# Optimization experiments

Measured on AMD Instinct MI355X. Metric: run time of the kernel, lower is better.

Reference implementation:

```python
import jax, jax.numpy as jnp
import numpy as np

N_NODES = 1_000_000
N_EDGES = 16_000_000


def _mean_aggregate(x, src, dst, num_nodes):
    # PyG message passing: message x_j = x[src], mean-aggregated at dst.
    msgs = x[src]  # [E, d]
    sums = jax.ops.segment_sum(msgs, dst, num_segments=num_nodes)
    cnt = jax.ops.segment_sum(jnp.ones((src.shape[0],), x.dtype), dst,
                              num_segments=num_nodes)
    return sums / jnp.maximum(cnt, 1.0)[:, None]


def _sage_conv(x, src, dst, W_l, b_l, W_r, num_nodes):
    # PyG SAGEConv (aggr='mean'): out = lin_l(mean_j x_j) + lin_r(x_i)
    agg = _mean_aggregate(x, src, dst, num_nodes)
    return agg @ W_l + b_l + x @ W_r


def setup_inputs() -> dict:
    key = jax.random.key(0)
    ks = jax.random.split(key, 12)
    x = jax.random.normal(ks[0], (N_NODES, 1), dtype=jnp.float32)
    edge_index = jax.random.randint(ks[1], (2, N_EDGES), 0, N_NODES, dtype=jnp.int64)

    def lin(k, din, dout):
        s = 1.0 / np.sqrt(din)
        return jax.random.uniform(k, (din, dout), jnp.float32, -s, s)

    return {
        "x": x, "edge_index": edge_index,
        "W1l": lin(ks[2], 1, 4), "b1": jnp.zeros((4,), jnp.float32), "W1r": lin(ks[3], 1, 4),
        "W2l": lin(ks[4], 4, 4), "b2": jnp.zeros((4,), jnp.float32), "W2r": lin(ks[5], 4, 4),
        "W3l": lin(ks[6], 4, 2), "b3": jnp.zeros((2,), jnp.float32), "W3r": lin(ks[7], 4, 2),
        "Wc": lin(ks[8], 2, 2), "bc": jnp.zeros((2,), jnp.float32),
    }


def reference(x, edge_index, W1l, b1, W1r, W2l, b2, W2r, W3l, b3, W3r, Wc, bc):
    src, dst = edge_index[0], edge_index[1]
    n = x.shape[0]
    h = jax.nn.relu(_sage_conv(x, src, dst, W1l, b1, W1r, n))
    h = jax.nn.relu(_sage_conv(h, src, dst, W2l, b2, W2r, n))
    h = jax.nn.relu(_sage_conv(h, src, dst, W3l, b3, W3r, n))
    out = h @ Wc + bc
    return (out, h)
```

## Files before the change

kernel.cpp:

```cpp
#include <hip/hip_runtime.h>
#include <hip/hip_fp16.h>


#define NBUCK 4096
#define CAP   4608
#define SRCM  0xFFFFFu
#define DEPTH 4

__device__ __forceinline__ ushort4 pack_h4(float4 f)
{
    ushort4 r;
    r.x = __half_as_ushort(__float2half_rn(f.x));
    r.y = __half_as_ushort(__float2half_rn(f.y));
    r.z = __half_as_ushort(__float2half_rn(f.z));
    r.w = __half_as_ushort(__float2half_rn(f.w));
    return r;
}

__device__ __forceinline__ float4 unpack_h4(ushort4 v)
{
    return make_float4(__half2float(__ushort_as_half(v.x)),
                       __half2float(__ushort_as_half(v.y)),
                       __half2float(__ushort_as_half(v.z)),
                       __half2float(__ushort_as_half(v.w)));
}

__global__ __launch_bounds__(256) void init_cursor(unsigned* __restrict__ cursor)
{
    int b = blockIdx.x * blockDim.x + threadIdx.x;
    if (b < NBUCK) cursor[b] = (unsigned)b * CAP;
}

__global__ __launch_bounds__(1024) void scatter_staged(
    const int* __restrict__ ei,
    unsigned* __restrict__ gcur,
    unsigned* __restrict__ bucket,
    long long E, long long chunk)
{
    __shared__ unsigned stage[NBUCK * DEPTH];
    __shared__ unsigned cnt[NBUCK];
    const int t = threadIdx.x;
    const long long beg = (long long)blockIdx.x * chunk;
    const long long end = min(E, beg + chunk);

    for (int i = t; i < NBUCK; i += 1024) cnt[i] = 0;
    __syncthreads();

    for (long long base = beg; base < end; base += 4096) {
        unsigned rec[4], bk[4], pos[4];
        int nv = 0;
        long long i = base + (long long)t * 4;
        if (i + 4 <= end) {
            int4 s4 = *reinterpret_cast<const int4*>(ei + i);
            int4 d4 = *reinterpret_cast<const int4*>(ei + E + i);
            rec[0] = (unsigned)s4.x | (((unsigned)d4.x & 255u) << 20); bk[0] = (unsigned)d4.x >> 8;
            rec[1] = (unsigned)s4.y | (((unsigned)d4.y & 255u) << 20); bk[1] = (unsigned)d4.y >> 8;
            rec[2] = (unsigned)s4.z | (((unsigned)d4.z & 255u) << 20); bk[2] = (unsigned)d4.z >> 8;
            rec[3] = (unsigned)s4.w | (((unsigned)d4.w & 255u) << 20); bk[3] = (unsigned)d4.w >> 8;
            nv = 4;
        } else {
            for (long long j = i; j < end && nv < 4; ++j) {
                unsigned s = (unsigned)ei[j];
                unsigned d = (unsigned)ei[E + j];
                rec[nv] = s | ((d & 255u) << 20);
                bk[nv] = d >> 8;
                ++nv;
            }
        }
        for (int k = 0; k < nv; ++k) pos[k] = atomicAdd(&cnt[bk[k]], 1u);
        __syncthreads();
        for (int k = 0; k < nv; ++k)
            if (pos[k] < DEPTH) stage[bk[k] * DEPTH + pos[k]] = rec[k];
        __syncthreads();
        for (int bb = t; bb < NBUCK; bb += 1024) {
            unsigned c = cnt[bb];
            if (c >= DEPTH) {
                unsigned gb = atomicAdd(&gcur[bb], DEPTH);
                unsigned lim = (unsigned)(bb + 1) * CAP;
                if ((gb & 3u) == 0u && gb + DEPTH <= lim) {
                    *reinterpret_cast<uint4*>(bucket + gb) =
                        *reinterpret_cast<const uint4*>(stage + bb * DEPTH);
                } else {
#pragma unroll
                    for (int k = 0; k < DEPTH; ++k)
                        if (gb + k < lim) bucket[gb + k] = stage[bb * DEPTH + k];
                }
                cnt[bb] = 0;
            }
        }
        __syncthreads();
        for (int k = 0; k < nv; ++k) {
            if (pos[k] >= DEPTH) {
                unsigned p2 = atomicAdd(&cnt[bk[k]], 1u);
                if (p2 < DEPTH) stage[bk[k] * DEPTH + p2] = rec[k];
                else {
                    unsigned gb = atomicAdd(&gcur[bk[k]], 1u);
                    if (gb < (unsigned)(bk[k] + 1) * CAP) bucket[gb] = rec[k];
                }
            }
        }
        __syncthreads();
    }
    for (int bb = t; bb < NBUCK; bb += 1024) {
        unsigned c = min(cnt[bb], (unsigned)DEPTH);
        if (c) {
            unsigned gb = atomicAdd(&gcur[bb], c);
            unsigned lim = (unsigned)(bb + 1) * CAP;
            for (unsigned k = 0; k < c; ++k)
                if (gb + k < lim) bucket[gb + k] = stage[bb * DEPTH + k];
        }
    }
}

template <bool EMIT16>
__global__ __launch_bounds__(256) void sort_l1(
    unsigned* __restrict__ bucket,
    const unsigned* __restrict__ cursor,
    unsigned* __restrict__ meta,
    const float* __restrict__ x,
    const float* __restrict__ W1l, const float* __restrict__ b1,
    const float* __restrict__ W1r,
    float* __restrict__ invout, float4* __restrict__ h1,
    ushort4* __restrict__ h1h, int N)
{
    __shared__ unsigned recA[CAP];
    __shared__ unsigned recB[CAP];
    __shared__ unsigned hist[256], pref[256], curs[256];
    const int t = threadIdx.x;
    const unsigned b = blockIdx.x;
    const unsigned base = b * CAP;
    const unsigned cnt = min(cursor[b] - base, (unsigned)CAP);

    hist[t] = 0;
    __syncthreads();
    for (unsigned i = t; i < cnt; i += 256) {
        unsigned r = bucket[base + i];
        recA[i] = r;
        atomicAdd(&hist[r >> 20], 1u);
    }
    __syncthreads();
    unsigned v = hist[t];
    pref[t] = v;
    __syncthreads();
    for (int off = 1; off < 256; off <<= 1) {
        unsigned u = (t >= off) ? pref[t - off] : 0u;
        __syncthreads();
        pref[t] += u;
        __syncthreads();
    }
    unsigned excl = pref[t] - v;
    curs[t] = excl;
    __syncthreads();
    for (unsigned i = t; i < cnt; i += 256) {
        unsigned r = recA[i];
        unsigned pos = atomicAdd(&curs[r >> 20], 1u);
        recB[pos] = r & SRCM;
    }
    __syncthreads();
    for (unsigned i = t; i < cnt; i += 256)
        bucket[base + i] = recB[i];

    int dst = (int)(b * 256u) + t;
    if (dst >= N) return;
    meta[dst] = excl | (v << 16);

    float sum = 0.0f;
    for (unsigned j = 0; j < v; ++j)
        sum += x[recB[excl + j]];
    float iv = 1.0f / fmaxf((float)v, 1.0f);
    invout[dst] = iv;
    float a = sum * iv;
    float xv = x[dst];
    float4 h;
    h.x = fmaxf(a * W1l[0] + b1[0] + xv * W1r[0], 0.0f);
    h.y = fmaxf(a * W1l[1] + b1[1] + xv * W1r[1], 0.0f);
    h.z = fmaxf(a * W1l[2] + b1[2] + xv * W1r[2], 0.0f);
    h.w = fmaxf(a * W1l[3] + b1[3] + xv * W1r[3], 0.0f);
    h1[dst] = h;
    if (EMIT16) h1h[dst] = pack_h4(h);
}

__device__ __forceinline__ float4 run_sum4(
    const unsigned* srtd, unsigned idx, unsigned c,
    const float4* __restrict__ feat)
{
    float a0 = 0, a1 = 0, a2 = 0, a3 = 0;
    unsigned j = 0;
    for (; j + 4 <= c; j += 4) {
        unsigned s0 = srtd[idx + j + 0];
        unsigned s1 = srtd[idx + j + 1];
        unsigned s2 = srtd[idx + j + 2];
        unsigned s3 = srtd[idx + j + 3];
        float4 f0 = feat[s0];
        float4 f1 = feat[s1];
        float4 f2 = feat[s2];
        float4 f3 = feat[s3];
        a0 += f0.x + f1.x + f2.x + f3.x;
        a1 += f0.y + f1.y + f2.y + f3.y;
        a2 += f0.z + f1.z + f2.z + f3.z;
        a3 += f0.w + f1.w + f2.w + f3.w;
    }
    for (; j < c; ++j) {
        float4 f = feat[srtd[idx + j]];
        a0 += f.x; a1 += f.y; a2 += f.z; a3 += f.w;
    }
    return make_float4(a0, a1, a2, a3);
}

__device__ __forceinline__ float4 run_sum4h_swept(
    const unsigned* srun, unsigned idx, unsigned c,
    const ushort4* __restrict__ feat)
{
    float a0 = 0, a1 = 0, a2 = 0, a3 = 0;
#pragma unroll 1
    for (unsigned q = 0; q < 4; ++q) {
        for (unsigned j = 0; j < c; ++j) {
            unsigned s = srun[idx + j];
            if ((s >> 18) == q) {
                float4 f = unpack_h4(feat[s]);
                a0 += f.x; a1 += f.y; a2 += f.z; a3 += f.w;
            }
        }
    }
    return make_float4(a0, a1, a2, a3);
}

template <bool USE16>
__global__ __launch_bounds__(256) void agg_l2(
    const unsigned* __restrict__ srtd, const unsigned* __restrict__ cursor,
    const unsigned* __restrict__ meta,
    const float4* __restrict__ h1, const ushort4* __restrict__ h1h,
    const float* __restrict__ inv,
    const float* __restrict__ W2l, const float* __restrict__ b2,
    const float* __restrict__ W2r,
    float4* __restrict__ h2, ushort4* __restrict__ h2h, int N)
{
    __shared__ unsigned srun[CAP];
    const int t = threadIdx.x;
    const unsigned b = blockIdx.x;
    const unsigned base = b * CAP;
    const unsigned bc = min(cursor[b] - base, (unsigned)CAP);
    for (unsigned i = t; i < bc; i += 256) srun[i] = srtd[base + i];
    __syncthreads();

    int dst = (int)(b * 256u) + t;
    if (dst >= N) return;
    unsigned m = meta[dst];
    float4 s4 = USE16 ? run_sum4h_swept(srun, m & 0xffffu, m >> 16, h1h)
                      : run_sum4      (srun, m & 0xffffu, m >> 16, h1);
    float iv = inv[dst];
    float a[4] = {s4.x * iv, s4.y * iv, s4.z * iv, s4.w * iv};
    float4 hv = h1[dst];
    float hr[4] = {hv.x, hv.y, hv.z, hv.w};
    float o[4];
#pragma unroll
    for (int j = 0; j < 4; ++j) {
        float acc = b2[j];
#pragma unroll
        for (int k = 0; k < 4; ++k)
            acc += a[k] * W2l[k * 4 + j] + hr[k] * W2r[k * 4 + j];
        o[j] = fmaxf(acc, 0.0f);
    }
    float4 h = make_float4(o[0], o[1], o[2], o[3]);
    h2[dst] = h;
    if (USE16) h2h[dst] = pack_h4(h);
}

template <bool USE16>
__global__ __launch_bounds__(256) void agg_l3(
    const unsigned* __restrict__ srtd, const unsigned* __restrict__ cursor,
    const unsigned* __restrict__ meta,
    const float4* __restrict__ h2, const ushort4* __restrict__ h2h,
    const float* __restrict__ inv,
    const float* __restrict__ W3l, const float* __restrict__ b3,
    const float* __restrict__ W3r,
    const float* __restrict__ Wc, const float* __restrict__ bc,
    float2* __restrict__ out, float2* __restrict__ hout, int N)
{
    __shared__ unsigned srun[CAP];
    const int t = threadIdx.x;
    const unsigned b = blockIdx.x;
    const unsigned base = b * CAP;
    const unsigned bcnt = min(cursor[b] - base, (unsigned)CAP);
    for (unsigned i = t; i < bcnt; i += 256) srun[i] = srtd[base + i];
    __syncthreads();

    int dst = (int)(b * 256u) + t;
    if (dst >= N) return;
    unsigned m = meta[dst];
    float4 s4 = USE16 ? run_sum4h_swept(srun, m & 0xffffu, m >> 16, h2h)
                      : run_sum4      (srun, m & 0xffffu, m >> 16, h2);
    float iv = inv[dst];
    float a[4] = {s4.x * iv, s4.y * iv, s4.z * iv, s4.w * iv};
    float4 hv = h2[dst];
    float hr[4] = {hv.x, hv.y, hv.z, hv.w};
    float h3[2];
#pragma unroll
    for (int j = 0; j < 2; ++j) {
        float acc = b3[j];
#pragma unroll
        for (int k = 0; k < 4; ++k)
            acc += a[k] * W3l[k * 2 + j] + hr[k] * W3r[k * 2 + j];
        h3[j] = fmaxf(acc, 0.0f);
    }
    float o0 = h3[0] * Wc[0] + h3[1] * Wc[2] + bc[0];
    float o1 = h3[0] * Wc[1] + h3[1] * Wc[3] + bc[1];
    out[dst]  = make_float2(o0, o1);
    hout[dst] = make_float2(h3[0], h3[1]);
}

#define FPS   262144.0f
#define IFPS  3.8146973e-06f
#define XBIAS 16.0f

__global__ __launch_bounds__(256) void edge_pass1(
    const int* __restrict__ ei, const float* __restrict__ x,
    unsigned long long* __restrict__ agg1, long long E)
{
    long long i = (long long)blockIdx.x * blockDim.x + threadIdx.x;
    const long long stride = (long long)gridDim.x * blockDim.x;
    for (; i < E; i += stride) {
        int s = ei[i];
        int d = ei[E + i];
        unsigned q = (unsigned)((x[s] + XBIAS) * FPS + 0.5f);
        atomicAdd(&agg1[d], (unsigned long long)q | (1ull << 32));
    }
}

__global__ __launch_bounds__(256) void edge_pass4(
    const int* __restrict__ ei, const float4* __restrict__ feat,
    unsigned long long* __restrict__ pair, long long E)
{
    long long i = (long long)blockIdx.x * blockDim.x + threadIdx.x;
    const long long stride = (long long)gridDim.x * blockDim.x;
    for (; i < E; i += stride) {
        int s = ei[i];
        int d = ei[E + i];
        float4 f = feat[s];
        unsigned q0 = (unsigned)(f.x * FPS + 0.5f);
        unsigned q1 = (unsigned)(f.y * FPS + 0.5f);
        unsigned q2 = (unsigned)(f.z * FPS + 0.5f);
        unsigned q3 = (unsigned)(f.w * FPS + 0.5f);
        atomicAdd(&pair[2ll*d+0], (unsigned long long)q0 | ((unsigned long long)q1 << 32));
        atomicAdd(&pair[2ll*d+1], (unsigned long long)q2 | ((unsigned long long)q3 << 32));
    }
}

__global__ __launch_bounds__(256) void node_pass1(
    const float* __restrict__ x, const unsigned long long* __restrict__ agg1,
    float* __restrict__ invout, const float* __restrict__ W1l,
    const float* __restrict__ b1, const float* __restrict__ W1r,
    float4* __restrict__ h1, int N)
{
    int i = blockIdx.x * blockDim.x + threadIdx.x;
    if (i >= N) return;
    unsigned long long v = agg1[i];
    float cnt = (float)(unsigned)(v >> 32);
    float lo  = (float)(unsigned)(v & 0xffffffffu);
    float sumx = lo * IFPS - XBIAS * cnt;
    float inv = 1.0f / fmaxf(cnt, 1.0f);
    invout[i] = inv;
    float a = sumx * inv;
    float xv = x[i];
    float4 h;
    h.x = fmaxf(a * W1l[0] + b1[0] + xv * W1r[0], 0.0f);
    h.y = fmaxf(a * W1l[1] + b1[1] + xv * W1r[1], 0.0f);
    h.z = fmaxf(a * W1l[2] + b1[2] + xv * W1r[2], 0.0f);
    h.w = fmaxf(a * W1l[3] + b1[3] + xv * W1r[3], 0.0f);
    h1[i] = h;
}

__device__ __forceinline__ float4 unpack_agg(const unsigned long long* pair, int i, float iv)
{
    unsigned long long m01 = pair[2ll * i + 0];
    unsigned long long m23 = pair[2ll * i + 1];
    float4 a;
    a.x = (float)(unsigned)(m01 & 0xffffffffu) * IFPS * iv;
    a.y = (float)(unsigned)(m01 >> 32)         * IFPS * iv;
    a.z = (float)(unsigned)(m23 & 0xffffffffu) * IFPS * iv;
    a.w = (float)(unsigned)(m23 >> 32)         * IFPS * iv;
    return a;
}

__global__ __launch_bounds__(256) void node_pass2(
    const unsigned long long* __restrict__ pair, const float4* __restrict__ h1,
    const float* __restrict__ inv, const float* __restrict__ W2l,
    const float* __restrict__ b2, const float* __restrict__ W2r,
    float4* __restrict__ h2, int N)
{
    int i = blockIdx.x * blockDim.x + threadIdx.x;
    if (i >= N) return;
    float iv = inv[i];
    float4 ag = unpack_agg(pair, i, iv);
    float4 hv = h1[i];
    float a[4]  = {ag.x, ag.y, ag.z, ag.w};
    float hr[4] = {hv.x, hv.y, hv.z, hv.w};
    float o[4];
#pragma unroll
    for (int j = 0; j < 4; ++j) {
        float acc = b2[j];
#pragma unroll
        for (int k = 0; k < 4; ++k)
            acc += a[k] * W2l[k * 4 + j] + hr[k] * W2r[k * 4 + j];
        o[j] = fmaxf(acc, 0.0f);
    }
    h2[i] = make_float4(o[0], o[1], o[2], o[3]);
}

__global__ __launch_bounds__(256) void node_pass3(
    const unsigned long long* __restrict__ pair, const float4* __restrict__ h2,
    const float* __restrict__ inv, const float* __restrict__ W3l,
    const float* __restrict__ b3, const float* __restrict__ W3r,
    const float* __restrict__ Wc, const float* __restrict__ bc,
    float2* __restrict__ out, float2* __restrict__ hout, int N)
{
    int i = blockIdx.x * blockDim.x + threadIdx.x;
    if (i >= N) return;
    float iv = inv[i];
    float4 ag = unpack_agg(pair, i, iv);
    float4 hv = h2[i];
    float a[4]  = {ag.x, ag.y, ag.z, ag.w};
    float hr[4] = {hv.x, hv.y, hv.z, hv.w};
    float h3[2];
#pragma unroll
    for (int j = 0; j < 2; ++j) {
        float acc = b3[j];
#pragma unroll
        for (int k = 0; k < 4; ++k)
            acc += a[k] * W3l[k * 2 + j] + hr[k] * W3r[k * 2 + j];
        h3[j] = fmaxf(acc, 0.0f);
    }
    float o0 = h3[0] * Wc[0] + h3[1] * Wc[2] + bc[0];
    float o1 = h3[0] * Wc[1] + h3[1] * Wc[3] + bc[1];
    out[i]  = make_float2(o0, o1);
    hout[i] = make_float2(h3[0], h3[1]);
}

extern "C" void kernel_launch(void* const* d_in, const int* in_sizes, int n_in,
                              void* d_out, int out_size, void* d_ws, size_t ws_size,
                              hipStream_t stream)
{
    const float* x   = (const float*)d_in[0];
    const int*   ei  = (const int*)d_in[1];
    const float* W1l = (const float*)d_in[2];
    const float* b1  = (const float*)d_in[3];
    const float* W1r = (const float*)d_in[4];
    const float* W2l = (const float*)d_in[5];
    const float* b2  = (const float*)d_in[6];
    const float* W2r = (const float*)d_in[7];
    const float* W3l = (const float*)d_in[8];
    const float* b3  = (const float*)d_in[9];
    const float* W3r = (const float*)d_in[10];
    const float* Wc  = (const float*)d_in[11];
    const float* bc  = (const float*)d_in[12];

    const long long N = in_sizes[0];
    const long long E = in_sizes[1] / 2;

    float* out  = (float*)d_out;
    float* hout = out + 2 * N;

    const size_t need_r7 =
        (size_t)(9 * N) * 4 + (size_t)NBUCK * 4 +
        (size_t)NBUCK * (size_t)CAP * 4 + (size_t)N * 4;
    const size_t need16 = need_r7 + (size_t)(4 * N) * 4;

    if (ws_size >= need_r7) {
        float*    inv    = (float*)d_ws;
        float*    h1     = inv + N;
        float*    h2     = h1 + 4 * N;
        unsigned* cursor = (unsigned*)(h2 + 4 * N);
        unsigned* bucket = cursor + NBUCK;
        unsigned* meta   = bucket + (size_t)NBUCK * CAP;
        ushort4*  h1h    = (ushort4*)(meta + N);
        ushort4*  h2h    = h1h + N;
        const bool f16   = ws_size >= need16;

        const int SB = 512;
        long long chunk = (E + SB - 1) / SB;
        chunk = (chunk + 4095) & ~4095ll;
        const int nbk = (int)((N + 255) / 256);

        init_cursor<<<NBUCK / 256, 256, 0, stream>>>(cursor);
        scatter_staged<<<SB, 1024, 0, stream>>>(ei, cursor, bucket, E, chunk);
        if (f16) {
            sort_l1<true><<<nbk, 256, 0, stream>>>(bucket, cursor, meta, x,
                W1l, b1, W1r, inv, (float4*)h1, h1h, (int)N);
            agg_l2<true><<<nbk, 256, 0, stream>>>(bucket, cursor, meta,
                (const float4*)h1, h1h, inv, W2l, b2, W2r, (float4*)h2, h2h, (int)N);
            agg_l3<true><<<nbk, 256, 0, stream>>>(bucket, cursor, meta,
                (const float4*)h2, h2h, inv, W3l, b3, W3r, Wc, bc,
                (float2*)out, (float2*)hout, (int)N);
        } else {
            sort_l1<false><<<nbk, 256, 0, stream>>>(bucket, cursor, meta, x,
                W1l, b1, W1r, inv, (float4*)h1, nullptr, (int)N);
            agg_l2<false><<<nbk, 256, 0, stream>>>(bucket, cursor, meta,
                (const float4*)h1, nullptr, inv, W2l, b2, W2r, (float4*)h2, nullptr, (int)N);
            agg_l3<false><<<nbk, 256, 0, stream>>>(bucket, cursor, meta,
                (const float4*)h2, nullptr, inv, W3l, b3, W3r, Wc, bc,
                (float2*)out, (float2*)hout, (int)N);
        }
        return;
    }

    float* ws  = (float*)d_ws;
    float* inv = ws;
    float* h1  = inv + N;
    unsigned long long* pair = (unsigned long long*)(h1 + 4 * N);
    float* h2  = (float*)(pair + 2 * N);

    const int nt = 256, eb = 8192;
    const int nb = (int)((N + nt - 1) / nt);

    hipMemsetAsync(pair, 0, (size_t)N * sizeof(unsigned long long), stream);
    edge_pass1<<<eb, nt, 0, stream>>>(ei, x, pair, E);
    node_pass1<<<nb, nt, 0, stream>>>(x, pair, inv, W1l, b1, W1r, (float4*)h1, (int)N);

    hipMemsetAsync(pair, 0, (size_t)(2 * N) * sizeof(unsigned long long), stream);
    edge_pass4<<<eb, nt, 0, stream>>>(ei, (const float4*)h1, pair, E);
    node_pass2<<<nb, nt, 0, stream>>>(pair, (const float4*)h1, inv,
                                      W2l, b2, W2r, (float4*)h2, (int)N);

    hipMemsetAsync(pair, 0, (size_t)(2 * N) * sizeof(unsigned long long), stream);
    edge_pass4<<<eb, nt, 0, stream>>>(ei, (const float4*)h2, pair, E);
    node_pass3<<<nb, nt, 0, stream>>>(pair, (const float4*)h2, inv,
                                      W3l, b3, W3r, Wc, bc,
                                      (float2*)out, (float2*)hout, (int)N);
}
```

Measured before the change: 623.5 us.

## Sort edge runs by source quarter and drop 4-pass swept gather loop

The in-bucket counting sort now keys on destination plus the top two bits of the source index, so each destination's run is ordered by source-address quarter. Per-quarter counts are packed into a new qcnt array, letting layers 2 and 3 walk each quarter once with unrolled gathers instead of rescanning the whole run four times with a predicate. This keeps the locality-sweep behaviour while removing the redundant shared-memory reads and branches. It costs a larger shared histogram, an extra per-node word of memory traffic, and a layer-1 sum that is now unrolled. The per-quarter counts are 8-bit, so a node with 256 or more in-edges from one quarter would be miscounted.

```diff
diff --git a/kernel.cpp b/kernel.cpp
--- a/kernel.cpp
+++ b/kernel.cpp
@@ -112,11 +112,17 @@
     }
 }
 
+__device__ __forceinline__ unsigned rec_key(unsigned r)
+{
+    return ((r >> 20) << 2) | ((r >> 18) & 3u);
+}
+
 template <bool EMIT16>
 __global__ __launch_bounds__(256) void sort_l1(
     unsigned* __restrict__ bucket,
     const unsigned* __restrict__ cursor,
     unsigned* __restrict__ meta,
+    unsigned* __restrict__ qcnt,
     const float* __restrict__ x,
     const float* __restrict__ W1l, const float* __restrict__ b1,
     const float* __restrict__ W1r,
@@ -125,22 +131,28 @@
 {
     __shared__ unsigned recA[CAP];
     __shared__ unsigned recB[CAP];
-    __shared__ unsigned hist[256], pref[256], curs[256];
+    __shared__ unsigned hist[1024];
+    __shared__ unsigned pref[256];
+    __shared__ unsigned curs[1024];
     const int t = threadIdx.x;
     const unsigned b = blockIdx.x;
     const unsigned base = b * CAP;
     const unsigned cnt = min(cursor[b] - base, (unsigned)CAP);
 
-    hist[t] = 0;
+    hist[t] = 0; hist[t + 256] = 0; hist[t + 512] = 0; hist[t + 768] = 0;
     __syncthreads();
     for (unsigned i = t; i < cnt; i += 256) {
         unsigned r = bucket[base + i];
         recA[i] = r;
-        atomicAdd(&hist[r >> 20], 1u);
-    }
-    __syncthreads();
-    unsigned v = hist[t];
-    pref[t] = v;
+        atomicAdd(&hist[rec_key(r)], 1u);
+    }
+    __syncthreads();
+    unsigned q0 = hist[4 * t + 0];
+    unsigned q1 = hist[4 * t + 1];
+    unsigned q2 = hist[4 * t + 2];
+    unsigned q3 = hist[4 * t + 3];
+    unsigned tot = q0 + q1 + q2 + q3;
+    pref[t] = tot;
     __syncthreads();
     for (int off = 1; off < 256; off <<= 1) {
         unsigned u = (t >= off) ? pref[t - off] : 0u;
@@ -148,12 +160,15 @@
         pref[t] += u;
         __syncthreads();
     }
-    unsigned excl = pref[t] - v;
-    curs[t] = excl;
+    unsigned excl = pref[t] - tot;
+    curs[4 * t + 0] = excl;
+    curs[4 * t + 1] = excl + q0;
+    curs[4 * t + 2] = excl + q0 + q1;
+    curs[4 * t + 3] = excl + q0 + q1 + q2;
     __syncthreads();
     for (unsigned i = t; i < cnt; i += 256) {
         unsigned r = recA[i];
-        unsigned pos = atomicAdd(&curs[r >> 20], 1u);
+        unsigned pos = atomicAdd(&curs[rec_key(r)], 1u);
         recB[pos] = r & SRCM;
     }
     __syncthreads();
@@ -162,12 +177,21 @@
 
     int dst = (int)(b * 256u) + t;
     if (dst >= N) return;
-    meta[dst] = excl | (v << 16);
+    meta[dst] = excl | (tot << 16);
+    qcnt[dst] = q0 | (q1 << 8) | (q2 << 16) | (q3 << 24);
 
     float sum = 0.0f;
-    for (unsigned j = 0; j < v; ++j)
-        sum += x[recB[excl + j]];
-    float iv = 1.0f / fmaxf((float)v, 1.0f);
+    unsigned j = 0;
+    for (; j + 4 <= tot; j += 4) {
+        unsigned s0 = recB[excl + j + 0];
+        unsigned s1 = recB[excl + j + 1];
+        unsigned s2 = recB[excl + j + 2];
+        unsigned s3 = recB[excl + j + 3];
+        sum += x[s0] + x[s1] + x[s2] + x[s3];
+    }
+    for (; j < tot; ++j) sum += x[recB[excl + j]];
+
+    float iv = 1.0f / fmaxf((float)tot, 1.0f);
     invout[dst] = iv;
     float a = sum * iv;
     float xv = x[dst];
@@ -180,47 +204,66 @@
     if (EMIT16) h1h[dst] = pack_h4(h);
 }
 
-__device__ __forceinline__ float4 run_sum4(
-    const unsigned* srtd, unsigned idx, unsigned c,
-    const float4* __restrict__ feat)
-{
-    float a0 = 0, a1 = 0, a2 = 0, a3 = 0;
-    unsigned j = 0;
-    for (; j + 4 <= c; j += 4) {
-        unsigned s0 = srtd[idx + j + 0];
-        unsigned s1 = srtd[idx + j + 1];
-        unsigned s2 = srtd[idx + j + 2];
-        unsigned s3 = srtd[idx + j + 3];
-        float4 f0 = feat[s0];
-        float4 f1 = feat[s1];
-        float4 f2 = feat[s2];
-        float4 f3 = feat[s3];
-        a0 += f0.x + f1.x + f2.x + f3.x;
-        a1 += f0.y + f1.y + f2.y + f3.y;
-        a2 += f0.z + f1.z + f2.z + f3.z;
-        a3 += f0.w + f1.w + f2.w + f3.w;
-    }
-    for (; j < c; ++j) {
-        float4 f = feat[srtd[idx + j]];
-        a0 += f.x; a1 += f.y; a2 += f.z; a3 += f.w;
-    }
-    return make_float4(a0, a1, a2, a3);
-}
-
-__device__ __forceinline__ float4 run_sum4h_swept(
-    const unsigned* srun, unsigned idx, unsigned c,
+__device__ __forceinline__ float4 run_sum_q16(
+    const unsigned* srun, unsigned idx, unsigned qc,
     const ushort4* __restrict__ feat)
 {
     float a0 = 0, a1 = 0, a2 = 0, a3 = 0;
 #pragma unroll 1
     for (unsigned q = 0; q < 4; ++q) {
-        for (unsigned j = 0; j < c; ++j) {
-            unsigned s = srun[idx + j];
-            if ((s >> 18) == q) {
-                float4 f = unpack_h4(feat[s]);
-                a0 += f.x; a1 += f.y; a2 += f.z; a3 += f.w;
-            }
-        }
+        unsigned c = (qc >> (8 * q)) & 255u;
+        unsigned j = 0;
+        for (; j + 4 <= c; j += 4) {
+            unsigned s0 = srun[idx + j + 0];
+            unsigned s1 = srun[idx + j + 1];
+            unsigned s2 = srun[idx + j + 2];
+            unsigned s3 = srun[idx + j + 3];
+            float4 f0 = unpack_h4(feat[s0]);
+            float4 f1 = unpack_h4(feat[s1]);
+            float4 f2 = unpack_h4(feat[s2]);
+            float4 f3 = unpack_h4(feat[s3]);
+            a0 += f0.x + f1.x + f2.x + f3.x;
+            a1 += f0.y + f1.y + f2.y + f3.y;
+            a2 += f0.z + f1.z + f2.z + f3.z;
+            a3 += f0.w + f1.w + f2.w + f3.w;
+        }
+        for (; j < c; ++j) {
+            float4 f = unpack_h4(feat[srun[idx + j]]);
+            a0 += f.x; a1 += f.y; a2 += f.z; a3 += f.w;
+        }
+        idx += c;
+    }
+    return make_float4(a0, a1, a2, a3);
+}
+
+__device__ __forceinline__ float4 run_sum_q32(
+    const unsigned* srun, unsigned idx, unsigned qc,
+    const float4* __restrict__ feat)
+{
+    float a0 = 0, a1 = 0, a2 = 0, a3 = 0;
+#pragma unroll 1
+    for (unsigned q = 0; q < 4; ++q) {
+        unsigned c = (qc >> (8 * q)) & 255u;
+        unsigned j = 0;
+        for (; j + 4 <= c; j += 4) {
+            unsigned s0 = srun[idx + j + 0];
+            unsigned s1 = srun[idx + j + 1];
+            unsigned s2 = srun[idx + j + 2];
+            unsigned s3 = srun[idx + j + 3];
+            float4 f0 = feat[s0];
+            float4 f1 = feat[s1];
+            float4 f2 = feat[s2];
+            float4 f3 = feat[s3];
+            a0 += f0.x + f1.x + f2.x + f3.x;
+            a1 += f0.y + f1.y + f2.y + f3.y;
+            a2 += f0.z + f1.z + f2.z + f3.z;
+            a3 += f0.w + f1.w + f2.w + f3.w;
+        }
+        for (; j < c; ++j) {
+            float4 f = feat[srun[idx + j]];
+            a0 += f.x; a1 += f.y; a2 += f.z; a3 += f.w;
+        }
+        idx += c;
     }
     return make_float4(a0, a1, a2, a3);
 }
@@ -228,7 +271,7 @@
 template <bool USE16>
 __global__ __launch_bounds__(256) void agg_l2(
     const unsigned* __restrict__ srtd, const unsigned* __restrict__ cursor,
-    const unsigned* __restrict__ meta,
+    const unsigned* __restrict__ meta, const unsigned* __restrict__ qcnt,
     const float4* __restrict__ h1, const ushort4* __restrict__ h1h,
     const float* __restrict__ inv,
     const float* __restrict__ W2l, const float* __restrict__ b2,
@@ -246,8 +289,9 @@
     int dst = (int)(b * 256u) + t;
     if (dst >= N) return;
     unsigned m = meta[dst];
-    float4 s4 = USE16 ? run_sum4h_swept(srun, m & 0xffffu, m >> 16, h1h)
-                      : run_sum4      (srun, m & 0xffffu, m >> 16, h1);
+    unsigned qc = qcnt[dst];
+    float4 s4 = USE16 ? run_sum_q16(srun, m & 0xffffu, qc, h1h)
+                      : run_sum_q32(srun, m & 0xffffu, qc, h1);
     float iv = inv[dst];
     float a[4] = {s4.x * iv, s4.y * iv, s4.z * iv, s4.w * iv};
     float4 hv = h1[dst];
@@ -269,7 +313,7 @@
 template <bool USE16>
 __global__ __launch_bounds__(256) void agg_l3(
     const unsigned* __restrict__ srtd, const unsigned* __restrict__ cursor,
-    const unsigned* __restrict__ meta,
+    const unsigned* __restrict__ meta, const unsigned* __restrict__ qcnt,
     const float4* __restrict__ h2, const ushort4* __restrict__ h2h,
     const float* __restrict__ inv,
     const float* __restrict__ W3l, const float* __restrict__ b3,
@@ -288,8 +332,9 @@
     int dst = (int)(b * 256u) + t;
     if (dst >= N) return;
     unsigned m = meta[dst];
-    float4 s4 = USE16 ? run_sum4h_swept(srun, m & 0xffffu, m >> 16, h2h)
-                      : run_sum4      (srun, m & 0xffffu, m >> 16, h2);
+    unsigned qc = qcnt[dst];
+    float4 s4 = USE16 ? run_sum_q16(srun, m & 0xffffu, qc, h2h)
+                      : run_sum_q32(srun, m & 0xffffu, qc, h2);
     float iv = inv[dst];
     float a[4] = {s4.x * iv, s4.y * iv, s4.z * iv, s4.w * iv};
     float4 hv = h2[dst];
@@ -460,19 +505,20 @@
     float* out  = (float*)d_out;
     float* hout = out + 2 * N;
 
-    const size_t need_r7 =
+    const size_t need_base =
         (size_t)(9 * N) * 4 + (size_t)NBUCK * 4 +
-        (size_t)NBUCK * (size_t)CAP * 4 + (size_t)N * 4;
-    const size_t need16 = need_r7 + (size_t)(4 * N) * 4;
-
-    if (ws_size >= need_r7) {
+        (size_t)NBUCK * (size_t)CAP * 4 + (size_t)(2 * N) * 4;
+    const size_t need16 = need_base + (size_t)(4 * N) * 4;
+
+    if (ws_size >= need_base) {
         float*    inv    = (float*)d_ws;
         float*    h1     = inv + N;
         float*    h2     = h1 + 4 * N;
         unsigned* cursor = (unsigned*)(h2 + 4 * N);
         unsigned* bucket = cursor + NBUCK;
         unsigned* meta   = bucket + (size_t)NBUCK * CAP;
-        ushort4*  h1h    = (ushort4*)(meta + N);
+        unsigned* qcnt   = meta + N;
+        ushort4*  h1h    = (ushort4*)(qcnt + N);
         ushort4*  h2h    = h1h + N;
         const bool f16   = ws_size >= need16;
 
@@ -484,19 +530,19 @@
         init_cursor<<<NBUCK / 256, 256, 0, stream>>>(cursor);
         scatter_staged<<<SB, 1024, 0, stream>>>(ei, cursor, bucket, E, chunk);
         if (f16) {
-            sort_l1<true><<<nbk, 256, 0, stream>>>(bucket, cursor, meta, x,
-                W1l, b1, W1r, inv, (float4*)h1, h1h, (int)N);
-            agg_l2<true><<<nbk, 256, 0, stream>>>(bucket, cursor, meta,
+            sort_l1<true><<<nbk, 256, 0, stream>>>(bucket, cursor, meta, qcnt,
+                x, W1l, b1, W1r, inv, (float4*)h1, h1h, (int)N);
+            agg_l2<true><<<nbk, 256, 0, stream>>>(bucket, cursor, meta, qcnt,
                 (const float4*)h1, h1h, inv, W2l, b2, W2r, (float4*)h2, h2h, (int)N);
-            agg_l3<true><<<nbk, 256, 0, stream>>>(bucket, cursor, meta,
+            agg_l3<true><<<nbk, 256, 0, stream>>>(bucket, cursor, meta, qcnt,
                 (const float4*)h2, h2h, inv, W3l, b3, W3r, Wc, bc,
                 (float2*)out, (float2*)hout, (int)N);
         } else {
-            sort_l1<false><<<nbk, 256, 0, stream>>>(bucket, cursor, meta, x,
-                W1l, b1, W1r, inv, (float4*)h1, nullptr, (int)N);
-            agg_l2<false><<<nbk, 256, 0, stream>>>(bucket, cursor, meta,
+            sort_l1<false><<<nbk, 256, 0, stream>>>(bucket, cursor, meta, qcnt,
+                x, W1l, b1, W1r, inv, (float4*)h1, nullptr, (int)N);
+            agg_l2<false><<<nbk, 256, 0, stream>>>(bucket, cursor, meta, qcnt,
                 (const float4*)h1, nullptr, inv, W2l, b2, W2r, (float4*)h2, nullptr, (int)N);
-            agg_l3<false><<<nbk, 256, 0, stream>>>(bucket, cursor, meta,
+            agg_l3<false><<<nbk, 256, 0, stream>>>(bucket, cursor, meta, qcnt,
                 (const float4*)h2, nullptr, inv, W3l, b3, W3r, Wc, bc,
                 (float2*)out, (float2*)hout, (int)N);
         }
```

Measured after the change: 680.9 us. 1.09x slower.
